# Optimization experiments

Hardware: AMD Instinct MI355X
Metric: run time of the kernel (lower is better)

## Reference

```python
import jax, jax.numpy as jnp
import numpy as np

T, H, E, K = 16384, 2880, 128, 4

def setup_inputs() -> dict:
    key = jax.random.key(0)
    k1, k2, k3 = jax.random.split(key, 3)
    return {
        "hidden_states": jax.random.normal(k1, (T, H), dtype=jnp.float32),
        "weight": jax.random.normal(k2, (E, H), dtype=jnp.float32) * 0.02,
        "bias": jax.random.normal(k3, (E,), dtype=jnp.float32) * 0.02,
    }

def reference(hidden_states, weight, bias):
    x = hidden_states.reshape(-1, weight.shape[1])            # [T, H]
    logits = jnp.einsum('th,eh->te', x, weight) + bias        # [T, E]
    top_val, top_idx = jax.lax.top_k(logits, K)               # sorted desc, [T, K]
    top_val = jax.nn.softmax(top_val, axis=-1)
    rows = jnp.arange(logits.shape[0])[:, None]
    scores = jnp.zeros_like(logits).at[rows, top_idx].set(top_val)
    return scores, top_idx
```

## Files before the change

kernel.cpp:

```cpp
#include <hip/hip_runtime.h>
#include <math.h>


#define T_TOK 16384
#define HDIM  2880
#define EEXP  128
#define KTOP  4

#define TM    32
#define NT    512
#define KCH   96
#define NPH   15
#define HALFK 1440
#define TAU   2.5e-4f

typedef __attribute__((ext_vector_type(8))) short bf16x8;
typedef __attribute__((ext_vector_type(4))) float f32x4;

#define MFMA(a, b, c) __builtin_amdgcn_mfma_f32_16x16x32_bf16((a), (b), (c), 0, 0, 0)

__global__ __launch_bounds__(256) void w_split(
    const float* __restrict__ w, char* __restrict__ wp)
{
    const int gid  = blockIdx.x * 256 + threadIdx.x;
    const int lane = gid & 63;
    const int q    = gid >> 6;
    const int c32  = q % 90;
    const int F    = q / 90;
    const int e    = F * 16 + (lane & 15);
    const int k0   = c32 * 32 + (lane >> 4) * 8;

    const float* src = w + (size_t)e * HDIM + k0;
    float4 v0 = *(const float4*)(src);
    float4 v1 = *(const float4*)(src + 4);
    float vv[8] = {v0.x, v0.y, v0.z, v0.w, v1.x, v1.y, v1.z, v1.w};
    union { unsigned short s[8]; uint4 u; } H, L;
#pragma unroll
    for (int j = 0; j < 8; ++j) {
        unsigned u = __float_as_uint(vv[j]);
        H.s[j] = (unsigned short)(u >> 16);
        float rr = vv[j] - __uint_as_float(u & 0xffff0000u);
        L.s[j] = (unsigned short)(__float_as_uint(rr) >> 16);
    }
    const int tile = (F * 90 + c32) * 2;
    *(uint4*)(wp + (size_t)tile * 1024 + lane * 16)       = H.u;
    *(uint4*)(wp + (size_t)(tile + 1) * 1024 + lane * 16) = L.u;
}

static __device__ __forceinline__ void split_write(char* base, int off, float4 v) {
    union { float4 v4; unsigned u[4]; } uv; uv.v4 = v;
    unsigned h01 = __builtin_amdgcn_perm(uv.u[1], uv.u[0], 0x07060302u);
    unsigned h23 = __builtin_amdgcn_perm(uv.u[3], uv.u[2], 0x07060302u);
    float r0 = v.x - __uint_as_float(uv.u[0] & 0xffff0000u);
    float r1 = v.y - __uint_as_float(uv.u[1] & 0xffff0000u);
    float r2 = v.z - __uint_as_float(uv.u[2] & 0xffff0000u);
    float r3 = v.w - __uint_as_float(uv.u[3] & 0xffff0000u);
    unsigned l01 = __builtin_amdgcn_perm(__float_as_uint(r1), __float_as_uint(r0), 0x07060302u);
    unsigned l23 = __builtin_amdgcn_perm(__float_as_uint(r3), __float_as_uint(r2), 0x07060302u);
    uint2 hw; hw.x = h01; hw.y = h23;
    uint2 lw; lw.x = l01; lw.y = l23;
    *(uint2*)(base + off)       = hw;
    *(uint2*)(base + off + 256) = lw;
}

__global__ __launch_bounds__(NT, 4) void router_fused(
    const float* __restrict__ x, const char* __restrict__ wp,
    const float* __restrict__ w, const float* __restrict__ bias,
    float* __restrict__ out)
{
    __shared__ char smem[65536];
    const int tid  = threadIdx.x;
    const int tok0 = blockIdx.x * TM;
    const int lane = tid & 63;
    const int wv   = tid >> 6;
    const int kt   = wv >> 2;
    const int wn   = wv & 3;
    const int r    = lane & 15;
    const int g    = lane >> 4;

    int hoff[3];
    const float* xptr[3];
#pragma unroll
    for (int i = 0; i < 3; ++i) {
        int f    = tid + i * NT;
        int half = (f >= 768) ? 1 : 0;
        int ff   = f - half * 768;
        int row  = ff / 24, c4 = ff % 24;
        int s    = c4 >> 1;
        hoff[i] = half * 32768 + row * 512 +
                  (((s ^ (row & 7)) << 4) | ((c4 & 1) << 3));
        xptr[i] = x + (size_t)(tok0 + row) * HDIM + half * HALFK + c4 * 4;
    }

    int aoff[2][3];
#pragma unroll
    for (int tf = 0; tf < 2; ++tf) {
        int row = tf * 16 + r;
#pragma unroll
        for (int ks = 0; ks < 3; ++ks) {
            int s = ks * 4 + g;
            aoff[tf][ks] = kt * 32768 + row * 512 + (((s ^ (row & 7)) << 4));
        }
    }

    f32x4 a00 = {0.f, 0.f, 0.f, 0.f}, a01 = a00, a10 = a00, a11 = a00;

#define LOADX(pf, cc) do {                                            \
        pf[0] = *(const float4*)(xptr[0] + (cc) * KCH);               \
        pf[1] = *(const float4*)(xptr[1] + (cc) * KCH);               \
        pf[2] = *(const float4*)(xptr[2] + (cc) * KCH); } while (0)

#define WRITEX(pf, cc) do { int bo_ = ((cc) & 1) * 16384;             \
        split_write(smem, hoff[0] + bo_, pf[0]);                      \
        split_write(smem, hoff[1] + bo_, pf[1]);                      \
        split_write(smem, hoff[2] + bo_, pf[2]); } while (0)

#define LOADW(W, cc) do {                                             \
        _Pragma("unroll")                                             \
        for (int ks_ = 0; ks_ < 3; ++ks_)                             \
        _Pragma("unroll")                                             \
        for (int F2_ = 0; F2_ < 2; ++F2_)                             \
        _Pragma("unroll")                                             \
        for (int p_ = 0; p_ < 2; ++p_) {                              \
            int c32_ = kt * 45 + (cc) * 3 + ks_;                      \
            int tile_ = ((wn * 2 + F2_) * 90 + c32_) * 2 + p_;        \
            W[ks_*4 + F2_*2 + p_] = *(const bf16x8*)(wp +             \
                (size_t)tile_ * 1024 + lane * 16);                    \
        } } while (0)

#define MFMA_CHUNK(bo, W) do {                                        \
        _Pragma("unroll")                                             \
        for (int ks_ = 0; ks_ < 3; ++ks_) {                           \
            bf16x8 ah0 = *(const bf16x8*)(smem + aoff[0][ks_] + (bo));\
            bf16x8 al0 = *(const bf16x8*)(smem + aoff[0][ks_] + (bo) + 256);\
            bf16x8 ah1 = *(const bf16x8*)(smem + aoff[1][ks_] + (bo));\
            bf16x8 al1 = *(const bf16x8*)(smem + aoff[1][ks_] + (bo) + 256);\
            bf16x8 bh0 = W[ks_*4], bl0 = W[ks_*4+1];                  \
            bf16x8 bh1 = W[ks_*4+2], bl1 = W[ks_*4+3];                \
            a00 = MFMA(ah0, bh0, a00); a01 = MFMA(ah0, bh1, a01);     \
            a10 = MFMA(ah1, bh0, a10); a11 = MFMA(ah1, bh1, a11);     \
            a00 = MFMA(ah0, bl0, a00); a01 = MFMA(ah0, bl1, a01);     \
            a10 = MFMA(ah1, bl0, a10); a11 = MFMA(ah1, bl1, a11);     \
            a00 = MFMA(al0, bh0, a00); a01 = MFMA(al0, bh1, a01);     \
            a10 = MFMA(al1, bh0, a10); a11 = MFMA(al1, bh1, a11);     \
        } } while (0)

    float4 pfA[3], pfB[3];
    bf16x8 W[12];

    LOADX(pfA, 0); LOADX(pfB, 1);
    WRITEX(pfA, 0);
    LOADX(pfA, 2);
    __syncthreads();

    for (int c = 0; c < 14; c += 2) {
        WRITEX(pfB, c + 1);
        if (c + 3 < NPH) LOADX(pfB, c + 3);
        LOADW(W, c);
        MFMA_CHUNK(0, W);
        __syncthreads();
        WRITEX(pfA, c + 2);
        if (c + 4 < NPH) LOADX(pfA, c + 4);
        LOADW(W, c + 1);
        MFMA_CHUNK(16384, W);
        __syncthreads();
    }
    LOADW(W, 14);
    MFMA_CHUNK(0, W);
    __syncthreads();

    float* red = (float*)smem;
    if (kt == 1) {
#pragma unroll
        for (int q = 0; q < 4; ++q) {
            int t0 = g * 4 + q, t1 = t0 + 16;
            red[(wn * 32 + t0) * 32 + r]      = a00[q];
            red[(wn * 32 + t0) * 32 + 16 + r] = a01[q];
            red[(wn * 32 + t1) * 32 + r]      = a10[q];
            red[(wn * 32 + t1) * 32 + 16 + r] = a11[q];
        }
    }
    __syncthreads();

    float* logitsL = (float*)(smem + 16384);
    if (kt == 0) {
        const float bv0 = bias[wn * 32 + r];
        const float bv1 = bias[wn * 32 + 16 + r];
#pragma unroll
        for (int q = 0; q < 4; ++q) {
            int t0 = g * 4 + q, t1 = t0 + 16;
            int e0 = wn * 32 + r, e1 = e0 + 16;
            logitsL[t0 * 130 + e0] = a00[q] + red[(wn * 32 + t0) * 32 + r]      + bv0;
            logitsL[t0 * 130 + e1] = a01[q] + red[(wn * 32 + t0) * 32 + 16 + r] + bv1;
            logitsL[t1 * 130 + e0] = a10[q] + red[(wn * 32 + t1) * 32 + r]      + bv0;
            logitsL[t1 * 130 + e1] = a11[q] + red[(wn * 32 + t1) * 32 + 16 + r] + bv1;
        }
    }
    float*  cvf = (float*) (smem + 33024);
    int*    cie = (int*)   (smem + 34048);
    int*    flg = (int*)   (smem + 35072);
    double* svd = (double*)(smem + 35200);
    int*    sid = (int*)   (smem + 36224);
    double* cvd = (double*)(smem + 36736);
    __syncthreads();

    if (tid < 256) {
        const int t = tid >> 3, s = tid & 7;
        float v[8]; int id[8];
#pragma unroll
        for (int k = 0; k < 8; ++k) { v[k] = -3.4e38f; id[k] = 0x7fffffff; }
        for (int jj = 0; jj < 16; ++jj) {
            float lv = logitsL[t * 130 + s * 16 + jj];
            int   e  = s * 16 + jj;
            bool gt[8];
#pragma unroll
            for (int k = 0; k < 8; ++k)
                gt[k] = (lv > v[k]) || (lv == v[k] && e < id[k]);
#pragma unroll
            for (int k = 7; k >= 1; --k)
                if (gt[k - 1]) { v[k] = v[k - 1]; id[k] = id[k - 1]; }
#pragma unroll
            for (int k = 0; k < 8; ++k) {
                bool put = gt[k] && (k == 0 || !gt[k - 1]);
                if (put) { v[k] = lv; id[k] = e; }
            }
        }
#pragma unroll
        for (int rd = 0; rd < 8; ++rd) {
            float hv = v[0]; int hi = id[0];
#pragma unroll
            for (int off = 1; off < 8; off <<= 1) {
                float ov = __shfl_xor(hv, off);
                int   oi = __shfl_xor(hi, off);
                if (ov > hv || (ov == hv && oi < hi)) { hv = ov; hi = oi; }
            }
            if (s == 0) { cvf[t * 8 + rd] = hv; cie[t * 8 + rd] = hi; }
            bool mine = (v[0] == hv) && (id[0] == hi);
            if (mine) {
#pragma unroll
                for (int k = 0; k < 7; ++k) { v[k] = v[k + 1]; id[k] = id[k + 1]; }
                v[7] = -3.4e38f; id[7] = 0x7fffffff;
            }
        }
    }
    __syncthreads();

    if (tid < TM) {
        float gmin = 3.4e38f;
#pragma unroll
        for (int k = 0; k < 4; ++k)
            gmin = fminf(gmin, cvf[tid * 8 + k] - cvf[tid * 8 + k + 1]);
        flg[tid] = (gmin < TAU);
    }
    if (tid < 128) {
        int t2 = tid >> 2, k = tid & 3;
        svd[t2 * 4 + k] = (double)cvf[t2 * 8 + k];
        sid[t2 * 4 + k] = cie[t2 * 8 + k];
    }
    __syncthreads();

    for (int ts = 0; ts < TM; ++ts) {
        if (!flg[ts]) continue;
        {
            const int ce = cie[ts * 8 + wv];
            const float4* xr = (const float4*)(x + (size_t)(tok0 + ts) * HDIM);
            const float4* wr = (const float4*)(w + (size_t)ce * HDIM);
            double q0 = 0.0, q1 = 0.0, q2 = 0.0, q3 = 0.0;
            for (int i2 = 0; i2 < 12; ++i2) {
                int fi = lane + i2 * 64;
                if (fi < HDIM / 4) {
                    float4 xv = xr[fi];
                    float4 wv4 = wr[fi];
                    q0 = fma((double)xv.x, (double)wv4.x, q0);
                    q1 = fma((double)xv.y, (double)wv4.y, q1);
                    q2 = fma((double)xv.z, (double)wv4.z, q2);
                    q3 = fma((double)xv.w, (double)wv4.w, q3);
                }
            }
            double accd = (q0 + q2) + (q1 + q3);
#pragma unroll
            for (int off = 32; off > 0; off >>= 1)
                accd += __shfl_xor(accd, off);
            if (lane == 0) cvd[wv] = accd + (double)bias[ce];
        }
        __syncthreads();
        if (tid < 8) {
            double mv = cvd[tid]; int mi2 = cie[ts * 8 + tid];
            int rk = 0;
#pragma unroll
            for (int j2 = 0; j2 < 8; ++j2) {
                double oj = cvd[j2];
                rk += (oj > mv) || (oj == mv && cie[ts * 8 + j2] < mi2);
            }
            if (rk < 4) { svd[ts * 4 + rk] = mv; sid[ts * 4 + rk] = mi2; }
        }
        __syncthreads();
    }

    float* srow = (float*)smem;
    float4 z4 = make_float4(0.f, 0.f, 0.f, 0.f);
#pragma unroll
    for (int i = 0; i < 2; ++i)
        ((float4*)srow)[tid + i * NT] = z4;
    __syncthreads();

    if (tid < TM) {
        double m  = svd[tid * 4];
        double e0 = exp(svd[tid * 4 + 0] - m), e1 = exp(svd[tid * 4 + 1] - m);
        double e2 = exp(svd[tid * 4 + 2] - m), e3 = exp(svd[tid * 4 + 3] - m);
        double inv = 1.0 / ((e0 + e1) + (e2 + e3));
        float* oidx = out + (size_t)T_TOK * EEXP + (size_t)(tok0 + tid) * KTOP;
        int i0 = sid[tid * 4 + 0], i1 = sid[tid * 4 + 1];
        int i2 = sid[tid * 4 + 2], i3 = sid[tid * 4 + 3];
        oidx[0] = (float)i0; oidx[1] = (float)i1;
        oidx[2] = (float)i2; oidx[3] = (float)i3;
        srow[tid * EEXP + i0] = (float)(e0 * inv);
        srow[tid * EEXP + i1] = (float)(e1 * inv);
        srow[tid * EEXP + i2] = (float)(e2 * inv);
        srow[tid * EEXP + i3] = (float)(e3 * inv);
    }
    __syncthreads();

    float4* orow = (float4*)(out + (size_t)tok0 * EEXP);
#pragma unroll
    for (int i = 0; i < 2; ++i)
        orow[tid + i * NT] = ((float4*)srow)[tid + i * NT];
}

extern "C" void kernel_launch(void* const* d_in, const int* in_sizes, int n_in,
                              void* d_out, int out_size, void* d_ws, size_t ws_size,
                              hipStream_t stream) {
    const float* x    = (const float*)d_in[0];
    const float* w    = (const float*)d_in[1];
    const float* bias = (const float*)d_in[2];
    float* out        = (float*)d_out;
    char*  wp         = (char*)d_ws;

    hipLaunchKernelGGL(w_split, dim3(180), dim3(256), 0, stream, w, wp);
    hipLaunchKernelGGL(router_fused, dim3(T_TOK / TM), dim3(NT), 0, stream,
                       x, wp, w, bias, out);
}
```

Measured before the change: 81.67 us.

## Drop LDS staging of x; split K four ways across waves with register MFMA operands

Removes the shared-memory double buffer for hidden states: each wave now loads x directly from global into registers, splits it into bf16 hi/lo, and feeds MFMA without LDS round-trips or per-chunk barriers. The K dimension is split across four wave groups (23/23/22/22 chunks of 32), each covering 64 experts, with partial sums reduced through a larger LDS region at the end. This cuts barrier and LDS traffic but makes each wave re-read its own x rows and weight tiles from global/L2, and raises LDS use to about 71 KB, which may reduce occupancy below the declared 4 blocks.

```diff
diff --git a/kernel.cpp b/kernel.cpp
--- a/kernel.cpp
+++ b/kernel.cpp
@@ -9,10 +9,17 @@
 
 #define TM    32
 #define NT    512
-#define KCH   96
-#define NPH   15
-#define HALFK 1440
 #define TAU   2.5e-4f
+
+#define PART_OFF   0
+#define LOGIT_OFF  50688
+#define CVF_OFF    67328
+#define CIE_OFF    68352
+#define FLG_OFF    69376
+#define SVD_OFF    69504
+#define SID_OFF    70528
+#define CVD_OFF    71040
+#define SMEM_SZ    71104
 
 typedef __attribute__((ext_vector_type(8))) short bf16x8;
 typedef __attribute__((ext_vector_type(4))) float f32x4;
@@ -47,20 +54,27 @@
     *(uint4*)(wp + (size_t)(tile + 1) * 1024 + lane * 16) = L.u;
 }
 
-static __device__ __forceinline__ void split_write(char* base, int off, float4 v) {
-    union { float4 v4; unsigned u[4]; } uv; uv.v4 = v;
-    unsigned h01 = __builtin_amdgcn_perm(uv.u[1], uv.u[0], 0x07060302u);
-    unsigned h23 = __builtin_amdgcn_perm(uv.u[3], uv.u[2], 0x07060302u);
-    float r0 = v.x - __uint_as_float(uv.u[0] & 0xffff0000u);
-    float r1 = v.y - __uint_as_float(uv.u[1] & 0xffff0000u);
-    float r2 = v.z - __uint_as_float(uv.u[2] & 0xffff0000u);
-    float r3 = v.w - __uint_as_float(uv.u[3] & 0xffff0000u);
-    unsigned l01 = __builtin_amdgcn_perm(__float_as_uint(r1), __float_as_uint(r0), 0x07060302u);
-    unsigned l23 = __builtin_amdgcn_perm(__float_as_uint(r3), __float_as_uint(r2), 0x07060302u);
-    uint2 hw; hw.x = h01; hw.y = h23;
-    uint2 lw; lw.x = l01; lw.y = l23;
-    *(uint2*)(base + off)       = hw;
-    *(uint2*)(base + off + 256) = lw;
+static __device__ __forceinline__ void split8(float4 v0, float4 v1,
+                                              bf16x8* h8, bf16x8* l8) {
+    union { float4 f; unsigned u[4]; } a, b; a.f = v0; b.f = v1;
+    union { unsigned u[4]; bf16x8 v; } H, L;
+    H.u[0] = __builtin_amdgcn_perm(a.u[1], a.u[0], 0x07060302u);
+    H.u[1] = __builtin_amdgcn_perm(a.u[3], a.u[2], 0x07060302u);
+    H.u[2] = __builtin_amdgcn_perm(b.u[1], b.u[0], 0x07060302u);
+    H.u[3] = __builtin_amdgcn_perm(b.u[3], b.u[2], 0x07060302u);
+    float r0 = v0.x - __uint_as_float(a.u[0] & 0xffff0000u);
+    float r1 = v0.y - __uint_as_float(a.u[1] & 0xffff0000u);
+    float r2 = v0.z - __uint_as_float(a.u[2] & 0xffff0000u);
+    float r3 = v0.w - __uint_as_float(a.u[3] & 0xffff0000u);
+    float r4 = v1.x - __uint_as_float(b.u[0] & 0xffff0000u);
+    float r5 = v1.y - __uint_as_float(b.u[1] & 0xffff0000u);
+    float r6 = v1.z - __uint_as_float(b.u[2] & 0xffff0000u);
+    float r7 = v1.w - __uint_as_float(b.u[3] & 0xffff0000u);
+    L.u[0] = __builtin_amdgcn_perm(__float_as_uint(r1), __float_as_uint(r0), 0x07060302u);
+    L.u[1] = __builtin_amdgcn_perm(__float_as_uint(r3), __float_as_uint(r2), 0x07060302u);
+    L.u[2] = __builtin_amdgcn_perm(__float_as_uint(r5), __float_as_uint(r4), 0x07060302u);
+    L.u[3] = __builtin_amdgcn_perm(__float_as_uint(r7), __float_as_uint(r6), 0x07060302u);
+    *h8 = H.v; *l8 = L.v;
 }
 
 __global__ __launch_bounds__(NT, 4) void router_fused(
@@ -68,140 +82,106 @@
     const float* __restrict__ w, const float* __restrict__ bias,
     float* __restrict__ out)
 {
-    __shared__ char smem[65536];
+    __shared__ char smem[SMEM_SZ];
     const int tid  = threadIdx.x;
     const int tok0 = blockIdx.x * TM;
     const int lane = tid & 63;
     const int wv   = tid >> 6;
-    const int kt   = wv >> 2;
-    const int wn   = wv & 3;
+    const int eh   = wv & 1;
+    const int kq   = wv >> 1;
     const int r    = lane & 15;
     const int g    = lane >> 4;
 
-    int hoff[3];
-    const float* xptr[3];
-#pragma unroll
-    for (int i = 0; i < 3; ++i) {
-        int f    = tid + i * NT;
-        int half = (f >= 768) ? 1 : 0;
-        int ff   = f - half * 768;
-        int row  = ff / 24, c4 = ff % 24;
-        int s    = c4 >> 1;
-        hoff[i] = half * 32768 + row * 512 +
-                  (((s ^ (row & 7)) << 4) | ((c4 & 1) << 3));
-        xptr[i] = x + (size_t)(tok0 + row) * HDIM + half * HALFK + c4 * 4;
-    }
-
-    int aoff[2][3];
-#pragma unroll
-    for (int tf = 0; tf < 2; ++tf) {
-        int row = tf * 16 + r;
-#pragma unroll
-        for (int ks = 0; ks < 3; ++ks) {
-            int s = ks * 4 + g;
-            aoff[tf][ks] = kt * 32768 + row * 512 + (((s ^ (row & 7)) << 4));
-        }
-    }
-
-    f32x4 a00 = {0.f, 0.f, 0.f, 0.f}, a01 = a00, a10 = a00, a11 = a00;
-
-#define LOADX(pf, cc) do {                                            \
-        pf[0] = *(const float4*)(xptr[0] + (cc) * KCH);               \
-        pf[1] = *(const float4*)(xptr[1] + (cc) * KCH);               \
-        pf[2] = *(const float4*)(xptr[2] + (cc) * KCH); } while (0)
-
-#define WRITEX(pf, cc) do { int bo_ = ((cc) & 1) * 16384;             \
-        split_write(smem, hoff[0] + bo_, pf[0]);                      \
-        split_write(smem, hoff[1] + bo_, pf[1]);                      \
-        split_write(smem, hoff[2] + bo_, pf[2]); } while (0)
-
-#define LOADW(W, cc) do {                                             \
+    const int c0 = (kq < 2) ? kq * 23 : 46 + (kq - 2) * 22;
+    const int c1 = c0 + ((kq < 2) ? 23 : 22);
+
+    const float* xp0 = x + (size_t)(tok0 + r) * HDIM + g * 8;
+    const float* xp1 = x + (size_t)(tok0 + 16 + r) * HDIM + g * 8;
+    const char* wbase = wp + lane * 16 + (size_t)(eh * 4) * 184320;
+
+    f32x4 acc[2][4];
+    const f32x4 zf = {0.f, 0.f, 0.f, 0.f};
+#pragma unroll
+    for (int tf = 0; tf < 2; ++tf)
+#pragma unroll
+        for (int ct = 0; ct < 4; ++ct) acc[tf][ct] = zf;
+
+#define LOADX(X, cc) do { int k_ = (cc) * 32;                         \
+        X[0] = *(const float4*)(xp0 + k_);                            \
+        X[1] = *(const float4*)(xp0 + k_ + 4);                        \
+        X[2] = *(const float4*)(xp1 + k_);                            \
+        X[3] = *(const float4*)(xp1 + k_ + 4); } while (0)
+
+#define COMPUTE(X, cc) do {                                           \
+        bf16x8 ah0, al0, ah1, al1;                                    \
+        split8(X[0], X[1], &ah0, &al0);                               \
+        split8(X[2], X[3], &ah1, &al1);                               \
+        const char* wc_ = wbase + (cc) * 2048;                        \
         _Pragma("unroll")                                             \
-        for (int ks_ = 0; ks_ < 3; ++ks_)                             \
-        _Pragma("unroll")                                             \
-        for (int F2_ = 0; F2_ < 2; ++F2_)                             \
-        _Pragma("unroll")                                             \
-        for (int p_ = 0; p_ < 2; ++p_) {                              \
-            int c32_ = kt * 45 + (cc) * 3 + ks_;                      \
-            int tile_ = ((wn * 2 + F2_) * 90 + c32_) * 2 + p_;        \
-            W[ks_*4 + F2_*2 + p_] = *(const bf16x8*)(wp +             \
-                (size_t)tile_ * 1024 + lane * 16);                    \
+        for (int ct_ = 0; ct_ < 4; ++ct_) {                           \
+            bf16x8 bh = *(const bf16x8*)(wc_ + ct_ * 184320);         \
+            bf16x8 bl = *(const bf16x8*)(wc_ + ct_ * 184320 + 1024);  \
+            acc[0][ct_] = MFMA(ah0, bh, acc[0][ct_]);                 \
+            acc[1][ct_] = MFMA(ah1, bh, acc[1][ct_]);                 \
+            acc[0][ct_] = MFMA(ah0, bl, acc[0][ct_]);                 \
+            acc[1][ct_] = MFMA(ah1, bl, acc[1][ct_]);                 \
+            acc[0][ct_] = MFMA(al0, bh, acc[0][ct_]);                 \
+            acc[1][ct_] = MFMA(al1, bh, acc[1][ct_]);                 \
         } } while (0)
 
-#define MFMA_CHUNK(bo, W) do {                                        \
-        _Pragma("unroll")                                             \
-        for (int ks_ = 0; ks_ < 3; ++ks_) {                           \
-            bf16x8 ah0 = *(const bf16x8*)(smem + aoff[0][ks_] + (bo));\
-            bf16x8 al0 = *(const bf16x8*)(smem + aoff[0][ks_] + (bo) + 256);\
-            bf16x8 ah1 = *(const bf16x8*)(smem + aoff[1][ks_] + (bo));\
-            bf16x8 al1 = *(const bf16x8*)(smem + aoff[1][ks_] + (bo) + 256);\
-            bf16x8 bh0 = W[ks_*4], bl0 = W[ks_*4+1];                  \
-            bf16x8 bh1 = W[ks_*4+2], bl1 = W[ks_*4+3];                \
-            a00 = MFMA(ah0, bh0, a00); a01 = MFMA(ah0, bh1, a01);     \
-            a10 = MFMA(ah1, bh0, a10); a11 = MFMA(ah1, bh1, a11);     \
-            a00 = MFMA(ah0, bl0, a00); a01 = MFMA(ah0, bl1, a01);     \
-            a10 = MFMA(ah1, bl0, a10); a11 = MFMA(ah1, bl1, a11);     \
-            a00 = MFMA(al0, bh0, a00); a01 = MFMA(al0, bh1, a01);     \
-            a10 = MFMA(al1, bh0, a10); a11 = MFMA(al1, bh1, a11);     \
-        } } while (0)
-
-    float4 pfA[3], pfB[3];
-    bf16x8 W[12];
-
-    LOADX(pfA, 0); LOADX(pfB, 1);
-    WRITEX(pfA, 0);
-    LOADX(pfA, 2);
-    __syncthreads();
-
-    for (int c = 0; c < 14; c += 2) {
-        WRITEX(pfB, c + 1);
-        if (c + 3 < NPH) LOADX(pfB, c + 3);
-        LOADW(W, c);
-        MFMA_CHUNK(0, W);
-        __syncthreads();
-        WRITEX(pfA, c + 2);
-        if (c + 4 < NPH) LOADX(pfA, c + 4);
-        LOADW(W, c + 1);
-        MFMA_CHUNK(16384, W);
-        __syncthreads();
-    }
-    LOADW(W, 14);
-    MFMA_CHUNK(0, W);
-    __syncthreads();
-
-    float* red = (float*)smem;
-    if (kt == 1) {
+    float4 xA[4], xB[4];
+    LOADX(xA, c0);
+    int c = c0;
+    while (c + 1 < c1) {
+        LOADX(xB, c + 1);
+        COMPUTE(xA, c);
+        if (c + 2 < c1) LOADX(xA, c + 2);
+        COMPUTE(xB, c + 1);
+        c += 2;
+    }
+    if (c < c1) COMPUTE(xA, c);
+
+    float* part = (float*)smem;
+    if (kq != 0) {
+        const int pb = (kq - 1) * 4224;
+#pragma unroll
+        for (int tf = 0; tf < 2; ++tf)
+#pragma unroll
+        for (int ct = 0; ct < 4; ++ct)
 #pragma unroll
         for (int q = 0; q < 4; ++q) {
-            int t0 = g * 4 + q, t1 = t0 + 16;
-            red[(wn * 32 + t0) * 32 + r]      = a00[q];
-            red[(wn * 32 + t0) * 32 + 16 + r] = a01[q];
-            red[(wn * 32 + t1) * 32 + r]      = a10[q];
-            red[(wn * 32 + t1) * 32 + 16 + r] = a11[q];
-        }
-    }
-    __syncthreads();
-
-    float* logitsL = (float*)(smem + 16384);
-    if (kt == 0) {
-        const float bv0 = bias[wn * 32 + r];
-        const float bv1 = bias[wn * 32 + 16 + r];
-#pragma unroll
-        for (int q = 0; q < 4; ++q) {
-            int t0 = g * 4 + q, t1 = t0 + 16;
-            int e0 = wn * 32 + r, e1 = e0 + 16;
-            logitsL[t0 * 130 + e0] = a00[q] + red[(wn * 32 + t0) * 32 + r]      + bv0;
-            logitsL[t0 * 130 + e1] = a01[q] + red[(wn * 32 + t0) * 32 + 16 + r] + bv1;
-            logitsL[t1 * 130 + e0] = a10[q] + red[(wn * 32 + t1) * 32 + r]      + bv0;
-            logitsL[t1 * 130 + e1] = a11[q] + red[(wn * 32 + t1) * 32 + 16 + r] + bv1;
-        }
-    }
-    float*  cvf = (float*) (smem + 33024);
-    int*    cie = (int*)   (smem + 34048);
-    int*    flg = (int*)   (smem + 35072);
-    double* svd = (double*)(smem + 35200);
-    int*    sid = (int*)   (smem + 36224);
-    double* cvd = (double*)(smem + 36736);
+            int tok = tf * 16 + g * 4 + q;
+            int e   = eh * 64 + ct * 16 + r;
+            part[pb + tok * 132 + e] = acc[tf][ct][q];
+        }
+    }
+    __syncthreads();
+
+    float* logitsL = (float*)(smem + LOGIT_OFF);
+    if (kq == 0) {
+#pragma unroll
+        for (int tf = 0; tf < 2; ++tf)
+#pragma unroll
+        for (int ct = 0; ct < 4; ++ct) {
+            int e = eh * 64 + ct * 16 + r;
+            float bv = bias[e];
+#pragma unroll
+            for (int q = 0; q < 4; ++q) {
+                int tok = tf * 16 + g * 4 + q;
+                float s = acc[tf][ct][q] + bv
+                        + part[0 * 4224 + tok * 132 + e]
+                        + part[1 * 4224 + tok * 132 + e]
+                        + part[2 * 4224 + tok * 132 + e];
+                logitsL[tok * 130 + e] = s;
+            }
+        }
+    }
+    float*  cvf = (float*) (smem + CVF_OFF);
+    int*    cie = (int*)   (smem + CIE_OFF);
+    int*    flg = (int*)   (smem + FLG_OFF);
+    double* svd = (double*)(smem + SVD_OFF);
+    int*    sid = (int*)   (smem + SID_OFF);
+    double* cvd = (double*)(smem + CVD_OFF);
     __syncthreads();
 
     if (tid < 256) {
```

Result: slower. 106.9 us (+30.9%).
